# Kernel optimization log

Hardware: AMD Instinct MI355X
Metric: run time of the kernel (lower is better)

The kernel has to match this reference:

```python
import jax, jax.numpy as jnp
import numpy as np


def setup_inputs() -> dict:
    key = jax.random.key(0)
    ks = jax.random.split(key, 7)
    B, C, H, W = 16, 256, 64, 64
    s = 1.0 / np.sqrt(C)  # ~kaiming-uniform scale for 1x1 conv
    return {
        "a": jax.random.normal(ks[0], (B, C, H, W), jnp.float32),
        "wq": jax.random.normal(ks[1], (C, C), jnp.float32) * s,
        "bq": jax.random.normal(ks[2], (C,), jnp.float32) * s,
        "wk": jax.random.normal(ks[3], (C, C), jnp.float32) * s,
        "bk": jax.random.normal(ks[4], (C,), jnp.float32) * s,
        "wv": jax.random.normal(ks[5], (C, C), jnp.float32) * s,
        "bv": jax.random.normal(ks[6], (C,), jnp.float32) * s,
    }


def reference(a, wq, bq, wk, bk, wv, bv):
    # 1x1 conv == per-pixel linear: [B,C,H,W] x [O,C] -> [B,H,W,O]
    def proj(w, b):
        return jnp.einsum('bchw,oc->bhwo', a, w) + b

    q = proj(wq, bq)  # [B,H,W,C]
    k = proj(wk, bk)
    v = proj(wv, bv)

    # unnormalized dot-product attention over the W axis, per row H
    attn = jnp.einsum('bhwc,bhxc->bhwx', q, k)       # [B,H,W,W]
    att_out = jnp.einsum('bhwx,bhxc->bhwc', attn, v)  # [B,H,W,C]

    # permute back to NCHW and residual add
    return a + jnp.transpose(att_out, (0, 3, 1, 2))
```

## Files before the change

### kernel.cpp

```cpp
#include <hip/hip_runtime.h>
#include <hip/hip_bf16.h>

#define NB 16
#define NC 256
#define NH 64
#define NW 64

typedef __attribute__((ext_vector_type(8))) short bf16x8;
typedef __attribute__((ext_vector_type(4))) float f32x4;

__device__ __forceinline__ unsigned short f2bf(float f) {
    union { float f; unsigned int u; } v; v.f = f;
    unsigned int u = v.u;
    u += 0x7fffu + ((u >> 16) & 1u);
    return (unsigned short)(u >> 16);
}

__device__ __forceinline__ int idxT(int row, int col) {
    return row * 256 + ((((col >> 3) ^ (row & 7)) << 3) | (col & 7));
}
__device__ __forceinline__ int idxS(int row, int col) {
    return row * 64 + ((((col >> 3) ^ (row & 7)) << 3) | (col & 7));
}

__global__ void conv_weights(const float* __restrict__ wq,
                             const float* __restrict__ wk,
                             const float* __restrict__ wv,
                             unsigned short* __restrict__ wsb) {
    int i = blockIdx.x * 256 + threadIdx.x;
    float4 q = ((const float4*)wq)[i];
    float4 k = ((const float4*)wk)[i];
    float4 v = ((const float4*)wv)[i];
    ushort4 uq = { f2bf(q.x), f2bf(q.y), f2bf(q.z), f2bf(q.w) };
    ushort4 uk = { f2bf(k.x), f2bf(k.y), f2bf(k.z), f2bf(k.w) };
    ushort4 uv = { f2bf(v.x), f2bf(v.y), f2bf(v.z), f2bf(v.w) };
    ((ushort4*)wsb)[i] = uq;
    ((ushort4*)(wsb + 65536))[i] = uk;
    ((ushort4*)(wsb + 131072))[i] = uv;
}

__launch_bounds__(512, 1)
__global__ void mha_fused(const float* __restrict__ a,
                          const unsigned short* __restrict__ wsb,
                          const float* __restrict__ bq,
                          const float* __restrict__ bk,
                          const float* __restrict__ bv,
                          float* __restrict__ out) {
    __shared__ __align__(16) unsigned short smem[69632];
    unsigned short* AL  = smem;
    unsigned short* QT  = smem;
    unsigned short* AT  = smem + 16384;
    unsigned short* KT  = smem + 32768;
    unsigned short* Vs  = smem + 49152;
    unsigned short* ATT = smem + 65536;

    const int tid = threadIdx.x;
    const int b = blockIdx.x >> 6;
    const int h = blockIdx.x & 63;
    const float* aB = a + (size_t)b * (NC * NH * NW) + h * NW;

    #pragma unroll
    for (int i = 0; i < 8; ++i) {
        int f = tid + i * 512;
        int c = f >> 4;
        int w4 = (f & 15) << 2;
        float4 val = *(const float4*)(aB + (size_t)c * (NH * NW) + w4);
        ushort4 u = { f2bf(val.x), f2bf(val.y), f2bf(val.z), f2bf(val.w) };
        *(ushort4*)(AL + c * 64 + w4) = u;
    }
    __syncthreads();

    {
        int w = tid & 63;
        int cg = tid >> 6;
        #pragma unroll
        for (int it = 0; it < 8; ++it) {
            int c0 = cg * 4 + it * 32;
            ushort4 t;
            t.x = AL[(c0 + 0) * 64 + w];
            t.y = AL[(c0 + 1) * 64 + w];
            t.z = AL[(c0 + 2) * 64 + w];
            t.w = AL[(c0 + 3) * 64 + w];
            *(ushort4*)(AT + idxT(w, c0)) = t;
        }
    }
    __syncthreads();

    const int wv_ = tid >> 6;
    const int lane = tid & 63;
    const int l15 = lane & 15;
    const int g = lane >> 4;

    {
        f32x4 acc[4][4];
        #pragma unroll
        for (int j = 0; j < 4; ++j) {
            int strip = wv_ * 4 + j;
            const float* bias = (strip < 16) ? bq : bk;
            float bvl = bias[((strip & 15) << 4) + l15];
            #pragma unroll
            for (int m = 0; m < 4; ++m)
                acc[j][m] = { bvl, bvl, bvl, bvl };
        }
        const unsigned short* wrow[4];
        #pragma unroll
        for (int j = 0; j < 4; ++j) {
            int strip = wv_ * 4 + j;
            const unsigned short* wb = (strip < 16) ? wsb : (wsb + 65536);
            wrow[j] = wb + (((strip & 15) << 4) + l15) * 256 + g * 8;
        }
        #pragma unroll
        for (int kk = 0; kk < 8; ++kk) {
            bf16x8 af[4], bfr[4];
            #pragma unroll
            for (int m = 0; m < 4; ++m) {
                int w = m * 16 + l15;
                af[m] = *(const bf16x8*)(AT + w * 256 + (((kk * 4 + g) ^ (w & 7)) << 3));
            }
            #pragma unroll
            for (int j = 0; j < 4; ++j)
                bfr[j] = *(const bf16x8*)(wrow[j] + kk * 32);
            #pragma unroll
            for (int j = 0; j < 4; ++j)
                #pragma unroll
                for (int m = 0; m < 4; ++m)
                    acc[j][m] = __builtin_amdgcn_mfma_f32_16x16x32_bf16(af[m], bfr[j], acc[j][m], 0, 0, 0);
        }
        #pragma unroll
        for (int j = 0; j < 4; ++j) {
            int strip = wv_ * 4 + j;
            unsigned short* T = (strip < 16) ? QT : KT;
            int o = ((strip & 15) << 4) + l15;
            #pragma unroll
            for (int m = 0; m < 4; ++m)
                #pragma unroll
                for (int r = 0; r < 4; ++r) {
                    int w = m * 16 + g * 4 + r;
                    T[idxT(w, o)] = f2bf(acc[j][m][r]);
                }
        }
    }

    {
        f32x4 acc[2][4];
        #pragma unroll
        for (int mi = 0; mi < 2; ++mi) {
            int m0 = (wv_ * 2 + mi) * 16;
            #pragma unroll
            for (int r = 0; r < 4; ++r) {
                float bvl = bv[m0 + g * 4 + r];
                #pragma unroll
                for (int n = 0; n < 4; ++n) acc[mi][n][r] = bvl;
            }
        }
        #pragma unroll
        for (int kk = 0; kk < 8; ++kk) {
            bf16x8 afw[2], bfa[4];
            #pragma unroll
            for (int mi = 0; mi < 2; ++mi) {
                int m0 = (wv_ * 2 + mi) * 16;
                afw[mi] = *(const bf16x8*)(wsb + 131072 + (m0 + l15) * 256 + kk * 32 + g * 8);
            }
            #pragma unroll
            for (int n = 0; n < 4; ++n) {
                int x = n * 16 + l15;
                bfa[n] = *(const bf16x8*)(AT + x * 256 + (((kk * 4 + g) ^ (x & 7)) << 3));
            }
            #pragma unroll
            for (int mi = 0; mi < 2; ++mi)
                #pragma unroll
                for (int n = 0; n < 4; ++n)
                    acc[mi][n] = __builtin_amdgcn_mfma_f32_16x16x32_bf16(afw[mi], bfa[n], acc[mi][n], 0, 0, 0);
        }
        #pragma unroll
        for (int mi = 0; mi < 2; ++mi)
            #pragma unroll
            for (int n = 0; n < 4; ++n)
                #pragma unroll
                for (int r = 0; r < 4; ++r) {
                    int c = (wv_ * 2 + mi) * 16 + g * 4 + r;
                    int x = n * 16 + l15;
                    Vs[idxS(c, x)] = f2bf(acc[mi][n][r]);
                }
    }
    __syncthreads();

    {
        f32x4 acc[2] = { { 0, 0, 0, 0 }, { 0, 0, 0, 0 } };
        int mt = wv_ >> 1;
        int wr = mt * 16 + l15;
        #pragma unroll
        for (int kk = 0; kk < 8; ++kk) {
            bf16x8 aq = *(const bf16x8*)(QT + wr * 256 + (((kk * 4 + g) ^ (wr & 7)) << 3));
            #pragma unroll
            for (int j = 0; j < 2; ++j) {
                int xr = ((wv_ & 1) * 2 + j) * 16 + l15;
                bf16x8 bkf = *(const bf16x8*)(KT + xr * 256 + (((kk * 4 + g) ^ (xr & 7)) << 3));
                acc[j] = __builtin_amdgcn_mfma_f32_16x16x32_bf16(aq, bkf, acc[j], 0, 0, 0);
            }
        }
        #pragma unroll
        for (int j = 0; j < 2; ++j) {
            int x = ((wv_ & 1) * 2 + j) * 16 + l15;
            #pragma unroll
            for (int r = 0; r < 4; ++r) {
                int w = mt * 16 + g * 4 + r;
                ATT[idxS(w, x)] = f2bf(acc[j][r]);
            }
        }
    }
    __syncthreads();

    {
        f32x4 acc[2][4];
        #pragma unroll
        for (int mi = 0; mi < 2; ++mi)
            #pragma unroll
            for (int n = 0; n < 4; ++n)
                acc[mi][n] = { 0.f, 0.f, 0.f, 0.f };
        #pragma unroll
        for (int kk = 0; kk < 2; ++kk) {
            bf16x8 av[2], bt[4];
            #pragma unroll
            for (int mi = 0; mi < 2; ++mi) {
                int c = (wv_ * 2 + mi) * 16 + l15;
                av[mi] = *(const bf16x8*)(Vs + c * 64 + (((kk * 4 + g) ^ (c & 7)) << 3));
            }
            #pragma unroll
            for (int n = 0; n < 4; ++n) {
                int w = n * 16 + l15;
                bt[n] = *(const bf16x8*)(ATT + w * 64 + (((kk * 4 + g) ^ (w & 7)) << 3));
            }
            #pragma unroll
            for (int mi = 0; mi < 2; ++mi)
                #pragma unroll
                for (int n = 0; n < 4; ++n)
                    acc[mi][n] = __builtin_amdgcn_mfma_f32_16x16x32_bf16(av[mi], bt[n], acc[mi][n], 0, 0, 0);
        }
        #pragma unroll
        for (int mi = 0; mi < 2; ++mi)
            #pragma unroll
            for (int n = 0; n < 4; ++n)
                #pragma unroll
                for (int r = 0; r < 4; ++r) {
                    int c = (wv_ * 2 + mi) * 16 + g * 4 + r;
                    int w = n * 16 + l15;
                    size_t off = (size_t)b * (NC * NH * NW) + (size_t)c * (NH * NW) + h * NW + w;
                    out[off] = a[off] + acc[mi][n][r];
                }
    }
}

extern "C" void kernel_launch(void* const* d_in, const int* in_sizes, int n_in,
                              void* d_out, int out_size, void* d_ws, size_t ws_size,
                              hipStream_t stream) {
    (void)in_sizes; (void)n_in; (void)out_size; (void)ws_size;
    const float* a  = (const float*)d_in[0];
    const float* wq = (const float*)d_in[1];
    const float* bq = (const float*)d_in[2];
    const float* wk = (const float*)d_in[3];
    const float* bk = (const float*)d_in[4];
    const float* wv = (const float*)d_in[5];
    const float* bv = (const float*)d_in[6];
    float* out = (float*)d_out;
    unsigned short* wsb = (unsigned short*)d_ws;

    conv_weights<<<dim3(64), dim3(256), 0, stream>>>(wq, wk, wv, wsb);
    mha_fused<<<dim3(NB * NH), dim3(512), 0, stream>>>(a, wsb, bq, bk, bv, out);
}
```

Measured before the change: 86.15 us.

## Chunk Q/K projection into attention accumulation to shrink LDS and raise occupancy

The full Q and K projections are no longer stored in shared memory. They are computed in 32-channel chunks, and each chunk's QK^T contribution is accumulated in registers right away. Swizzled layouts are replaced by padded strides, and the V/AL and Q/ATT regions now overlap, which cuts LDS from about 136KB to about 78KB so two blocks can share a CU. The launch bound is raised to ask for more resident waves. In exchange, the chunk loop adds 16 barriers and issues fewer MFMAs per barrier interval, and the tighter register budget could cause spills.

After: 162.9 us. 89.1% more time.

```diff
diff --git a/kernel.cpp b/kernel.cpp
--- a/kernel.cpp
+++ b/kernel.cpp
@@ -18,9 +18,6 @@
 
 __device__ __forceinline__ int idxT(int row, int col) {
     return row * 256 + ((((col >> 3) ^ (row & 7)) << 3) | (col & 7));
-}
-__device__ __forceinline__ int idxS(int row, int col) {
-    return row * 64 + ((((col >> 3) ^ (row & 7)) << 3) | (col & 7));
 }
 
 __global__ void conv_weights(const float* __restrict__ wq,
@@ -39,20 +36,28 @@
     ((ushort4*)(wsb + 131072))[i] = uv;
 }
 
-__launch_bounds__(512, 1)
+#define OFF_AV   16384
+#define OFF_QC   34816
+#define OFF_KC   37376
+#define OFF_ATT  34816
+#define VS_STR   72
+#define QC_STR   40
+#define ATT_STR  72
+
+__launch_bounds__(512, 4)
 __global__ void mha_fused(const float* __restrict__ a,
                           const unsigned short* __restrict__ wsb,
                           const float* __restrict__ bq,
                           const float* __restrict__ bk,
                           const float* __restrict__ bv,
                           float* __restrict__ out) {
-    __shared__ __align__(16) unsigned short smem[69632];
-    unsigned short* AL  = smem;
-    unsigned short* QT  = smem;
-    unsigned short* AT  = smem + 16384;
-    unsigned short* KT  = smem + 32768;
-    unsigned short* Vs  = smem + 49152;
-    unsigned short* ATT = smem + 65536;
+    __shared__ __align__(16) unsigned short smem[39936];
+    unsigned short* AT  = smem;
+    unsigned short* AL  = smem + OFF_AV;
+    unsigned short* Vs  = smem + OFF_AV;
+    unsigned short* Qc  = smem + OFF_QC;
+    unsigned short* Kc  = smem + OFF_KC;
+    unsigned short* ATT = smem + OFF_ATT;
 
     const int tid = threadIdx.x;
     const int b = blockIdx.x >> 6;
@@ -92,56 +97,6 @@
     const int g = lane >> 4;
 
     {
-        f32x4 acc[4][4];
-        #pragma unroll
-        for (int j = 0; j < 4; ++j) {
-            int strip = wv_ * 4 + j;
-            const float* bias = (strip < 16) ? bq : bk;
-            float bvl = bias[((strip & 15) << 4) + l15];
-            #pragma unroll
-            for (int m = 0; m < 4; ++m)
-                acc[j][m] = { bvl, bvl, bvl, bvl };
-        }
-        const unsigned short* wrow[4];
-        #pragma unroll
-        for (int j = 0; j < 4; ++j) {
-            int strip = wv_ * 4 + j;
-            const unsigned short* wb = (strip < 16) ? wsb : (wsb + 65536);
-            wrow[j] = wb + (((strip & 15) << 4) + l15) * 256 + g * 8;
-        }
-        #pragma unroll
-        for (int kk = 0; kk < 8; ++kk) {
-            bf16x8 af[4], bfr[4];
-            #pragma unroll
-            for (int m = 0; m < 4; ++m) {
-                int w = m * 16 + l15;
-                af[m] = *(const bf16x8*)(AT + w * 256 + (((kk * 4 + g) ^ (w & 7)) << 3));
-            }
-            #pragma unroll
-            for (int j = 0; j < 4; ++j)
-                bfr[j] = *(const bf16x8*)(wrow[j] + kk * 32);
-            #pragma unroll
-            for (int j = 0; j < 4; ++j)
-                #pragma unroll
-                for (int m = 0; m < 4; ++m)
-                    acc[j][m] = __builtin_amdgcn_mfma_f32_16x16x32_bf16(af[m], bfr[j], acc[j][m], 0, 0, 0);
-        }
-        #pragma unroll
-        for (int j = 0; j < 4; ++j) {
-            int strip = wv_ * 4 + j;
-            unsigned short* T = (strip < 16) ? QT : KT;
-            int o = ((strip & 15) << 4) + l15;
-            #pragma unroll
-            for (int m = 0; m < 4; ++m)
-                #pragma unroll
-                for (int r = 0; r < 4; ++r) {
-                    int w = m * 16 + g * 4 + r;
-                    T[idxT(w, o)] = f2bf(acc[j][m][r]);
-                }
-        }
-    }
-
-    {
         f32x4 acc[2][4];
         #pragma unroll
         for (int mi = 0; mi < 2; ++mi) {
@@ -180,33 +135,63 @@
                 for (int r = 0; r < 4; ++r) {
                     int c = (wv_ * 2 + mi) * 16 + g * 4 + r;
                     int x = n * 16 + l15;
-                    Vs[idxS(c, x)] = f2bf(acc[mi][n][r]);
+                    Vs[c * VS_STR + x] = f2bf(acc[mi][n][r]);
                 }
     }
-    __syncthreads();
-
-    {
-        f32x4 acc[2] = { { 0, 0, 0, 0 }, { 0, 0, 0, 0 } };
-        int mt = wv_ >> 1;
-        int wr = mt * 16 + l15;
+
+    f32x4 acc3[2] = { { 0, 0, 0, 0 }, { 0, 0, 0, 0 } };
+    const int mtq = wv_ & 1;
+    const int ntq = wv_ >> 1;
+    const int mt3 = wv_ >> 1;
+    const int xb  = (wv_ & 1) * 2;
+
+    #pragma unroll 1
+    for (int ch = 0; ch < 8; ++ch) {
+        const int o0 = ch * 32 + mtq * 16;
+        f32x4 accq, acck;
+        #pragma unroll
+        for (int r = 0; r < 4; ++r) {
+            accq[r] = bq[o0 + g * 4 + r];
+            acck[r] = bk[o0 + g * 4 + r];
+        }
+        const unsigned short* wqrow = wsb + (o0 + l15) * 256;
+        const unsigned short* wkrow = wsb + 65536 + (o0 + l15) * 256;
+        const int w = ntq * 16 + l15;
         #pragma unroll
         for (int kk = 0; kk < 8; ++kk) {
-            bf16x8 aq = *(const bf16x8*)(QT + wr * 256 + (((kk * 4 + g) ^ (wr & 7)) << 3));
+            bf16x8 awq = *(const bf16x8*)(wqrow + kk * 32 + g * 8);
+            bf16x8 awk = *(const bf16x8*)(wkrow + kk * 32 + g * 8);
+            bf16x8 bfa = *(const bf16x8*)(AT + w * 256 + (((kk * 4 + g) ^ (w & 7)) << 3));
+            accq = __builtin_amdgcn_mfma_f32_16x16x32_bf16(awq, bfa, accq, 0, 0, 0);
+            acck = __builtin_amdgcn_mfma_f32_16x16x32_bf16(awk, bfa, acck, 0, 0, 0);
+        }
+        {
+            ushort4 uq = { f2bf(accq[0]), f2bf(accq[1]), f2bf(accq[2]), f2bf(accq[3]) };
+            ushort4 uk = { f2bf(acck[0]), f2bf(acck[1]), f2bf(acck[2]), f2bf(acck[3]) };
+            *(ushort4*)(Qc + w * QC_STR + mtq * 16 + g * 4) = uq;
+            *(ushort4*)(Kc + w * QC_STR + mtq * 16 + g * 4) = uk;
+        }
+        __syncthreads();
+        {
+            const int wr = mt3 * 16 + l15;
+            bf16x8 aq = *(const bf16x8*)(Qc + wr * QC_STR + g * 8);
             #pragma unroll
             for (int j = 0; j < 2; ++j) {
-                int xr = ((wv_ & 1) * 2 + j) * 16 + l15;
-                bf16x8 bkf = *(const bf16x8*)(KT + xr * 256 + (((kk * 4 + g) ^ (xr & 7)) << 3));
-                acc[j] = __builtin_amdgcn_mfma_f32_16x16x32_bf16(aq, bkf, acc[j], 0, 0, 0);
-            }
-        }
-        #pragma unroll
-        for (int j = 0; j < 2; ++j) {
-            int x = ((wv_ & 1) * 2 + j) * 16 + l15;
-            #pragma unroll
-            for (int r = 0; r < 4; ++r) {
-                int w = mt * 16 + g * 4 + r;
-                ATT[idxS(w, x)] = f2bf(acc[j][r]);
-            }
+                const int xr = (xb + j) * 16 + l15;
+                bf16x8 bkf = *(const bf16x8*)(Kc + xr * QC_STR + g * 8);
+                acc3[j] = __builtin_amdgcn_mfma_f32_16x16x32_bf16(aq, bkf, acc3[j], 0, 0, 0);
+            }
+        }
+        __syncthreads();
+    }
+
+    #pragma unroll
+    for (int j = 0; j < 2; ++j) {
+        const int x = (xb + j) * 16 + l15;
+        #pragma unroll
+        for (int r = 0; r < 4; ++r) {
+            const int wrow = mt3 * 16 + g * 4 + r;
+            ATT[wrow * ATT_STR + x] = f2bf(acc3[j][r]);
         }
     }
     __syncthreads();
@@ -224,12 +209,12 @@
             #pragma unroll
             for (int mi = 0; mi < 2; ++mi) {
                 int c = (wv_ * 2 + mi) * 16 + l15;
-                av[mi] = *(const bf16x8*)(Vs + c * 64 + (((kk * 4 + g) ^ (c & 7)) << 3));
+                av[mi] = *(const bf16x8*)(Vs + c * VS_STR + kk * 32 + g * 8);
             }
             #pragma unroll
             for (int n = 0; n < 4; ++n) {
-                int w = n * 16 + l15;
-                bt[n] = *(const bf16x8*)(ATT + w * 64 + (((kk * 4 + g) ^ (w & 7)) << 3));
+                int wrow = n * 16 + l15;
+                bt[n] = *(const bf16x8*)(ATT + wrow * ATT_STR + kk * 32 + g * 8);
             }
             #pragma unroll
             for (int mi = 0; mi < 2; ++mi)
```

## Shrink LDS footprint, vectorize transposed stores, and allow two blocks per CU

Applied to the files above, without the earlier changes.

Loads the input tile and converts it straight into the transposed swizzled layout, dropping the intermediate LDS buffer and one barrier. Swaps MFMA operand order so accumulators hold contiguous output columns, which lets LDS writes become ushort4 and the final residual read and output write become float4. Reorders the stages so Q·K^T runs before the V projection and V and ATT reuse the Q/K regions, cutting LDS from ~136KB to 96KB. Launch bounds move to 2 blocks per CU for more occupancy, which limits registers per thread and adds an extra barrier.

After: 92.56 us. 7.4% more time.

```diff
diff --git a/kernel.cpp b/kernel.cpp
--- a/kernel.cpp
+++ b/kernel.cpp
@@ -14,13 +14,6 @@
     unsigned int u = v.u;
     u += 0x7fffu + ((u >> 16) & 1u);
     return (unsigned short)(u >> 16);
-}
-
-__device__ __forceinline__ int idxT(int row, int col) {
-    return row * 256 + ((((col >> 3) ^ (row & 7)) << 3) | (col & 7));
-}
-__device__ __forceinline__ int idxS(int row, int col) {
-    return row * 64 + ((((col >> 3) ^ (row & 7)) << 3) | (col & 7));
 }
 
 __global__ void conv_weights(const float* __restrict__ wq,
@@ -39,20 +32,19 @@
     ((ushort4*)(wsb + 131072))[i] = uv;
 }
 
-__launch_bounds__(512, 1)
+__launch_bounds__(512, 2)
 __global__ void mha_fused(const float* __restrict__ a,
                           const unsigned short* __restrict__ wsb,
                           const float* __restrict__ bq,
                           const float* __restrict__ bk,
                           const float* __restrict__ bv,
                           float* __restrict__ out) {
-    __shared__ __align__(16) unsigned short smem[69632];
-    unsigned short* AL  = smem;
-    unsigned short* QT  = smem;
-    unsigned short* AT  = smem + 16384;
+    __shared__ __align__(16) unsigned short smem[49152];
+    unsigned short* AT  = smem;
+    unsigned short* QT  = smem + 16384;
     unsigned short* KT  = smem + 32768;
-    unsigned short* Vs  = smem + 49152;
-    unsigned short* ATT = smem + 65536;
+    unsigned short* Vs  = smem + 16384;
+    unsigned short* ATT = smem + 32768;
 
     const int tid = threadIdx.x;
     const int b = blockIdx.x >> 6;
@@ -60,28 +52,23 @@
     const float* aB = a + (size_t)b * (NC * NH * NW) + h * NW;
 
     #pragma unroll
-    for (int i = 0; i < 8; ++i) {
-        int f = tid + i * 512;
-        int c = f >> 4;
-        int w4 = (f & 15) << 2;
-        float4 val = *(const float4*)(aB + (size_t)c * (NH * NW) + w4);
-        ushort4 u = { f2bf(val.x), f2bf(val.y), f2bf(val.z), f2bf(val.w) };
-        *(ushort4*)(AL + c * 64 + w4) = u;
-    }
-    __syncthreads();
-
-    {
-        int w = tid & 63;
-        int cg = tid >> 6;
-        #pragma unroll
-        for (int it = 0; it < 8; ++it) {
-            int c0 = cg * 4 + it * 32;
-            ushort4 t;
-            t.x = AL[(c0 + 0) * 64 + w];
-            t.y = AL[(c0 + 1) * 64 + w];
-            t.z = AL[(c0 + 2) * 64 + w];
-            t.w = AL[(c0 + 3) * 64 + w];
-            *(ushort4*)(AT + idxT(w, c0)) = t;
+    for (int half = 0; half < 2; ++half) {
+        int mt = tid + half * 512;
+        int c0 = (mt >> 4) << 2;
+        int w0 = (mt & 15) << 2;
+        float4 r0 = *(const float4*)(aB + (size_t)(c0 + 0) * 4096 + w0);
+        float4 r1 = *(const float4*)(aB + (size_t)(c0 + 1) * 4096 + w0);
+        float4 r2 = *(const float4*)(aB + (size_t)(c0 + 2) * 4096 + w0);
+        float4 r3 = *(const float4*)(aB + (size_t)(c0 + 3) * 4096 + w0);
+        const float* f0 = (const float*)&r0;
+        const float* f1 = (const float*)&r1;
+        const float* f2 = (const float*)&r2;
+        const float* f3 = (const float*)&r3;
+        #pragma unroll
+        for (int j = 0; j < 4; ++j) {
+            int w = w0 + j;
+            ushort4 u = { f2bf(f0[j]), f2bf(f1[j]), f2bf(f2[j]), f2bf(f3[j]) };
+            *(ushort4*)(AT + w * 256 + ((((c0 >> 3) ^ (w & 7)) << 3) | (c0 & 7))) = u;
         }
     }
     __syncthreads();
@@ -93,51 +80,78 @@
 
     {
         f32x4 acc[4][4];
+        const unsigned short* wrow[4];
         #pragma unroll
         for (int j = 0; j < 4; ++j) {
             int strip = wv_ * 4 + j;
             const float* bias = (strip < 16) ? bq : bk;
-            float bvl = bias[((strip & 15) << 4) + l15];
-            #pragma unroll
-            for (int m = 0; m < 4; ++m)
-                acc[j][m] = { bvl, bvl, bvl, bvl };
-        }
-        const unsigned short* wrow[4];
-        #pragma unroll
-        for (int j = 0; j < 4; ++j) {
-            int strip = wv_ * 4 + j;
             const unsigned short* wb = (strip < 16) ? wsb : (wsb + 65536);
-            wrow[j] = wb + (((strip & 15) << 4) + l15) * 256 + g * 8;
+            int o_l = (strip & 15) * 16;
+            wrow[j] = wb + (o_l + l15) * 256;
+            f32x4 bi = { bias[o_l + g * 4 + 0], bias[o_l + g * 4 + 1],
+                         bias[o_l + g * 4 + 2], bias[o_l + g * 4 + 3] };
+            #pragma unroll
+            for (int m = 0; m < 4; ++m) acc[j][m] = bi;
         }
         #pragma unroll
         for (int kk = 0; kk < 8; ++kk) {
-            bf16x8 af[4], bfr[4];
+            bf16x8 wf[4], atf[4];
+            #pragma unroll
+            for (int j = 0; j < 4; ++j)
+                wf[j] = *(const bf16x8*)(wrow[j] + kk * 32 + g * 8);
             #pragma unroll
             for (int m = 0; m < 4; ++m) {
                 int w = m * 16 + l15;
-                af[m] = *(const bf16x8*)(AT + w * 256 + (((kk * 4 + g) ^ (w & 7)) << 3));
-            }
-            #pragma unroll
-            for (int j = 0; j < 4; ++j)
-                bfr[j] = *(const bf16x8*)(wrow[j] + kk * 32);
+                atf[m] = *(const bf16x8*)(AT + w * 256 + (((kk * 4 + g) ^ (w & 7)) << 3));
+            }
             #pragma unroll
             for (int j = 0; j < 4; ++j)
                 #pragma unroll
                 for (int m = 0; m < 4; ++m)
-                    acc[j][m] = __builtin_amdgcn_mfma_f32_16x16x32_bf16(af[m], bfr[j], acc[j][m], 0, 0, 0);
+                    acc[j][m] = __builtin_amdgcn_mfma_f32_16x16x32_bf16(wf[j], atf[m], acc[j][m], 0, 0, 0);
         }
         #pragma unroll
         for (int j = 0; j < 4; ++j) {
             int strip = wv_ * 4 + j;
             unsigned short* T = (strip < 16) ? QT : KT;
-            int o = ((strip & 15) << 4) + l15;
-            #pragma unroll
-            for (int m = 0; m < 4; ++m)
-                #pragma unroll
-                for (int r = 0; r < 4; ++r) {
-                    int w = m * 16 + g * 4 + r;
-                    T[idxT(w, o)] = f2bf(acc[j][m][r]);
-                }
+            int o0 = (strip & 15) * 16 + g * 4;
+            #pragma unroll
+            for (int m = 0; m < 4; ++m) {
+                int w = m * 16 + l15;
+                ushort4 u = { f2bf(acc[j][m][0]), f2bf(acc[j][m][1]),
+                              f2bf(acc[j][m][2]), f2bf(acc[j][m][3]) };
+                *(ushort4*)(T + w * 256 + ((((o0 >> 3) ^ (w & 7)) << 3) | (o0 & 7))) = u;
+            }
+        }
+    }
+    __syncthreads();
+
+    f32x4 acc3[2] = { { 0, 0, 0, 0 }, { 0, 0, 0, 0 } };
+    const int wt3 = wv_ >> 1;
+    const int xb3 = (wv_ & 1) * 2;
+    {
+        const int w = wt3 * 16 + l15;
+        #pragma unroll
+        for (int kk = 0; kk < 8; ++kk) {
+            bf16x8 qf = *(const bf16x8*)(QT + w * 256 + (((kk * 4 + g) ^ (w & 7)) << 3));
+            #pragma unroll
+            for (int j = 0; j < 2; ++j) {
+                int x = (xb3 + j) * 16 + l15;
+                bf16x8 kf = *(const bf16x8*)(KT + x * 256 + (((kk * 4 + g) ^ (x & 7)) << 3));
+                acc3[j] = __builtin_amdgcn_mfma_f32_16x16x32_bf16(kf, qf, acc3[j], 0, 0, 0);
+            }
+        }
+    }
+    __syncthreads();
+
+    {
+        const int w = wt3 * 16 + l15;
+        #pragma unroll
+        for (int j = 0; j < 2; ++j) {
+            int x0 = (xb3 + j) * 16 + g * 4;
+            ushort4 u = { f2bf(acc3[j][0]), f2bf(acc3[j][1]),
+                          f2bf(acc3[j][2]), f2bf(acc3[j][3]) };
+            *(ushort4*)(ATT + w * 64 + ((((x0 >> 3) ^ (w & 7)) << 3) | (x0 & 7))) = u;
         }
     }
 
@@ -145,67 +159,39 @@
         f32x4 acc[2][4];
         #pragma unroll
         for (int mi = 0; mi < 2; ++mi) {
-            int m0 = (wv_ * 2 + mi) * 16;
-            #pragma unroll
-            for (int r = 0; r < 4; ++r) {
-                float bvl = bv[m0 + g * 4 + r];
-                #pragma unroll
-                for (int n = 0; n < 4; ++n) acc[mi][n][r] = bvl;
-            }
+            int c = (wv_ * 2 + mi) * 16 + l15;
+            float bvl = bv[c];
+            #pragma unroll
+            for (int n = 0; n < 4; ++n) acc[mi][n] = { bvl, bvl, bvl, bvl };
         }
         #pragma unroll
         for (int kk = 0; kk < 8; ++kk) {
-            bf16x8 afw[2], bfa[4];
+            bf16x8 wvf[2], atx[4];
             #pragma unroll
             for (int mi = 0; mi < 2; ++mi) {
-                int m0 = (wv_ * 2 + mi) * 16;
-                afw[mi] = *(const bf16x8*)(wsb + 131072 + (m0 + l15) * 256 + kk * 32 + g * 8);
+                int c = (wv_ * 2 + mi) * 16 + l15;
+                wvf[mi] = *(const bf16x8*)(wsb + 131072 + c * 256 + kk * 32 + g * 8);
             }
             #pragma unroll
             for (int n = 0; n < 4; ++n) {
                 int x = n * 16 + l15;
-                bfa[n] = *(const bf16x8*)(AT + x * 256 + (((kk * 4 + g) ^ (x & 7)) << 3));
+                atx[n] = *(const bf16x8*)(AT + x * 256 + (((kk * 4 + g) ^ (x & 7)) << 3));
             }
             #pragma unroll
             for (int mi = 0; mi < 2; ++mi)
                 #pragma unroll
                 for (int n = 0; n < 4; ++n)
-                    acc[mi][n] = __builtin_amdgcn_mfma_f32_16x16x32_bf16(afw[mi], bfa[n], acc[mi][n], 0, 0, 0);
-        }
-        #pragma unroll
-        for (int mi = 0; mi < 2; ++mi)
-            #pragma unroll
-            for (int n = 0; n < 4; ++n)
-                #pragma unroll
-                for (int r = 0; r < 4; ++r) {
-                    int c = (wv_ * 2 + mi) * 16 + g * 4 + r;
-                    int x = n * 16 + l15;
-                    Vs[idxS(c, x)] = f2bf(acc[mi][n][r]);
-                }
-    }
-    __syncthreads();
-
-    {
-        f32x4 acc[2] = { { 0, 0, 0, 0 }, { 0, 0, 0, 0 } };
-        int mt = wv_ >> 1;
-        int wr = mt * 16 + l15;
-        #pragma unroll
-        for (int kk = 0; kk < 8; ++kk) {
-            bf16x8 aq = *(const bf16x8*)(QT + wr * 256 + (((kk * 4 + g) ^ (wr & 7)) << 3));
-            #pragma unroll
-            for (int j = 0; j < 2; ++j) {
-                int xr = ((wv_ & 1) * 2 + j) * 16 + l15;
-                bf16x8 bkf = *(const bf16x8*)(KT + xr * 256 + (((kk * 4 + g) ^ (xr & 7)) << 3));
-                acc[j] = __builtin_amdgcn_mfma_f32_16x16x32_bf16(aq, bkf, acc[j], 0, 0, 0);
-            }
-        }
-        #pragma unroll
-        for (int j = 0; j < 2; ++j) {
-            int x = ((wv_ & 1) * 2 + j) * 16 + l15;
-            #pragma unroll
-            for (int r = 0; r < 4; ++r) {
-                int w = mt * 16 + g * 4 + r;
-                ATT[idxS(w, x)] = f2bf(acc[j][r]);
+                    acc[mi][n] = __builtin_amdgcn_mfma_f32_16x16x32_bf16(atx[n], wvf[mi], acc[mi][n], 0, 0, 0);
+        }
+        #pragma unroll
+        for (int mi = 0; mi < 2; ++mi) {
+            int c = (wv_ * 2 + mi) * 16 + l15;
+            #pragma unroll
+            for (int n = 0; n < 4; ++n) {
+                int x0 = n * 16 + g * 4;
+                ushort4 u = { f2bf(acc[mi][n][0]), f2bf(acc[mi][n][1]),
+                              f2bf(acc[mi][n][2]), f2bf(acc[mi][n][3]) };
+                *(ushort4*)(Vs + c * 64 + ((((x0 >> 3) ^ (c & 7)) << 3) | (x0 & 7))) = u;
             }
         }
     }
@@ -220,34 +206,41 @@
                 acc[mi][n] = { 0.f, 0.f, 0.f, 0.f };
         #pragma unroll
         for (int kk = 0; kk < 2; ++kk) {
-            bf16x8 av[2], bt[4];
+            bf16x8 attf[4], vsf[2];
+            #pragma unroll
+            for (int n = 0; n < 4; ++n) {
+                int w = n * 16 + l15;
+                attf[n] = *(const bf16x8*)(ATT + w * 64 + (((kk * 4 + g) ^ (w & 7)) << 3));
+            }
             #pragma unroll
             for (int mi = 0; mi < 2; ++mi) {
                 int c = (wv_ * 2 + mi) * 16 + l15;
-                av[mi] = *(const bf16x8*)(Vs + c * 64 + (((kk * 4 + g) ^ (c & 7)) << 3));
-            }
-            #pragma unroll
-            for (int n = 0; n < 4; ++n) {
-                int w = n * 16 + l15;
-                bt[n] = *(const bf16x8*)(ATT + w * 64 + (((kk * 4 + g) ^ (w & 7)) << 3));
+                vsf[mi] = *(const bf16x8*)(Vs + c * 64 + (((kk * 4 + g) ^ (c & 7)) << 3));
             }
             #pragma unroll
             for (int mi = 0; mi < 2; ++mi)
                 #pragma unroll
                 for (int n = 0; n < 4; ++n)
-                    acc[mi][n] = __builtin_amdgcn_mfma_f32_16x16x32_bf16(av[mi], bt[n], acc[mi][n], 0, 0, 0);
-        }
-        #pragma unroll
-        for (int mi = 0; mi < 2; ++mi)
-            #pragma unroll
-            for (int n = 0; n < 4; ++n)
-                #pragma unroll
-                for (int r = 0; r < 4; ++r) {
-                    int c = (wv_ * 2 + mi) * 16 + g * 4 + r;
-                    int w = n * 16 + l15;
-                    size_t off = (size_t)b * (NC * NH * NW) + (size_t)c * (NH * NW) + h * NW + w;
-                    out[off] = a[off] + acc[mi][n][r];
-                }
+                    acc[mi][n] = __builtin_amdgcn_mfma_f32_16x16x32_bf16(attf[n], vsf[mi], acc[mi][n], 0, 0, 0);
+        }
+        float* outB = out + (size_t)b * (NC * NH * NW) + h * NW;
+        #pragma unroll
+        for (int mi = 0; mi < 2; ++mi) {
+            int c = (wv_ * 2 + mi) * 16 + l15;
+            const float* ain = aB + (size_t)c * 4096;
+            float* po = outB + (size_t)c * 4096;
+            #pragma unroll
+            for (int n = 0; n < 4; ++n) {
+                int w0 = n * 16 + g * 4;
+                float4 res = *(const float4*)(ain + w0);
+                float4 o4;
+                o4.x = res.x + acc[mi][n][0];
+                o4.y = res.y + acc[mi][n][1];
+                o4.z = res.z + acc[mi][n][2];
+                o4.w = res.w + acc[mi][n][3];
+                *(float4*)(po + w0) = o4;
+            }
+        }
     }
 }
 
```
